# Performance work log

Measured on AMD Instinct MI355X. Metric: run time of the kernel, lower is better.

The kernel has to match this reference:

```python
import jax, jax.numpy as jnp
from jax import lax
import numpy as np

DN = ('NCDHW', 'OIDHW', 'NCDHW')
SLOPE = 0.01   # nn.LeakyReLU default negative_slope
EPS = 1e-5     # nn.BatchNorm1d default eps


def _conv(x, w, s, p):
    return lax.conv_general_dilated(x, w, (s, s, s), [(p, p)] * 3,
                                    dimension_numbers=DN)


def _tconv(x, w):
    # ConvTranspose3d(k=4, s=2, p=1) == conv with lhs_dilation=2,
    # pad = k-1-p = 2, spatially flipped kernel. w is (C_out, C_in, 4,4,4).
    return lax.conv_general_dilated(x, jnp.flip(w, (2, 3, 4)), (1, 1, 1),
                                    [(2, 2)] * 3, lhs_dilation=(2, 2, 2),
                                    dimension_numbers=DN)


def _bcast(v):
    return v[None, :, None, None, None]


def _masked_bn(y, m, g, b):
    # BatchNorm1d over ACTIVE voxels only (spconv stores only active sites).
    cnt = jnp.maximum(jnp.sum(m), 1.0)
    mean = jnp.sum(y * m, axis=(0, 2, 3, 4)) / cnt
    var = jnp.sum(jnp.square(y - _bcast(mean)) * m, axis=(0, 2, 3, 4)) / cnt
    yhat = (y - _bcast(mean)) * _bcast(lax.rsqrt(var + EPS))
    return (yhat * _bcast(g) + _bcast(b)) * m


def _block(x, m, w, b, g, be, transpose):
    # spconv SparseConv(Transpose)3d -> LeakyReLU -> BatchNorm1d, emulated
    # densely: x is zero off the active set m; output active set is the
    # dilation of m by the kernel footprint; bias/activation/BN touch only
    # active sites.
    ones_k = jnp.ones((1, 1, 4, 4, 4), x.dtype)
    if transpose:
        y = _tconv(x, w)
        m2 = (_tconv(m, ones_k) > 0).astype(x.dtype)
    else:
        y = _conv(x, w, 2, 1)
        m2 = (_conv(m, ones_k, 2, 1) > 0).astype(x.dtype)
    y = (y + _bcast(b)) * m2
    y = jnp.where(y >= 0, y, SLOPE * y)  # LeakyReLU (preserves zeros)
    return _masked_bn(y, m2, g, be), m2


def setup_inputs() -> dict:
    key = jax.random.key(0)
    ks = jax.random.split(key, 16)
    B, C, D = 2, 4, 64
    c = 32          # chans
    pred_dim = 32

    def w_init(k, shape):
        scale = 1.0 / float(np.sqrt(np.prod(shape[1:])))
        return jax.random.normal(k, shape, jnp.float32) * scale

    def b_init(k, n):
        return jax.random.normal(k, (n,), jnp.float32) * 0.01

    inp = {
        'feat': jax.random.normal(ks[0], (B, C, D, D, D), jnp.float32),
        'mask': jax.random.uniform(ks[1], (B, 1, D, D, D), jnp.float32),
        # down: [C->c, c->2c, 2c->4c], k=4 s=2 p=1
        'w1': w_init(ks[2], (c, C, 4, 4, 4)),
        'b1': b_init(ks[3], c),
        'g1': jnp.ones((c,), jnp.float32), 'be1': jnp.zeros((c,), jnp.float32),
        'w2': w_init(ks[4], (2 * c, c, 4, 4, 4)),
        'b2': b_init(ks[5], 2 * c),
        'g2': jnp.ones((2 * c,), jnp.float32), 'be2': jnp.zeros((2 * c,), jnp.float32),
        'w3': w_init(ks[6], (4 * c, 2 * c, 4, 4, 4)),
        'b3': b_init(ks[7], 4 * c),
        'g3': jnp.ones((4 * c,), jnp.float32), 'be3': jnp.zeros((4 * c,), jnp.float32),
        # up: [4c->4c, 4c->2c] (no skip-concat in the executed forward)
        'tw1': w_init(ks[8], (4 * c, 4 * c, 4, 4, 4)),
        'tb1': b_init(ks[9], 4 * c),
        'tg1': jnp.ones((4 * c,), jnp.float32), 'tbe1': jnp.zeros((4 * c,), jnp.float32),
        'tw2': w_init(ks[10], (2 * c, 4 * c, 4, 4, 4)),
        'tb2': b_init(ks[11], 2 * c),
        'tg2': jnp.ones((2 * c,), jnp.float32), 'tbe2': jnp.zeros((2 * c,), jnp.float32),
        # final dense 1x1x1 Conv3d: 2c -> pred_dim
        'fw': w_init(ks[12], (pred_dim, 2 * c, 1, 1, 1)),
        'fb': b_init(ks[13], pred_dim),
    }
    return inp


def reference(feat, mask, w1, b1, g1, be1, w2, b2, g2, be2, w3, b3, g3, be3,
              tw1, tb1, tg1, tbe1, tw2, tb2, tg2, tbe2, fw, fb):
    m = (mask > 0.5).astype(feat.dtype)
    x = feat * m  # gather of active voxel features == dense zero-fill
    x, m = _block(x, m, w1, b1, g1, be1, False)   # 64^3 -> 32^3
    x, m = _block(x, m, w2, b2, g2, be2, False)   # 32^3 -> 16^3
    x, m = _block(x, m, w3, b3, g3, be3, False)   # 16^3 -> 8^3
    x, m = _block(x, m, tw1, tb1, tg1, tbe1, True)  # 8^3 -> 16^3
    x, m = _block(x, m, tw2, tb2, tg2, tbe2, True)  # 16^3 -> 32^3
    # ToDense() then dense 1x1x1 Conv3d (bias applied everywhere)
    return _conv(x, fw, 1, 0) + _bcast(fb)
```

## Files before the change

### kernel.cpp

```cpp
#include <hip/hip_runtime.h>
#include <hip/hip_bf16.h>

#define DEV static __device__ __forceinline__

typedef unsigned short ushort;
typedef __attribute__((ext_vector_type(8))) short short8;
typedef __attribute__((ext_vector_type(8))) ushort ushort8;
typedef __attribute__((ext_vector_type(4))) ushort ushortx4;
typedef __attribute__((ext_vector_type(4))) float accv;

DEV ushort f2bf(float f) {
    __hip_bfloat16 h = __float2bfloat16(f);
    return reinterpret_cast<ushort&>(h);
}

__device__ float    g_sred[5 * 128 * 32];
__device__ float    g_y1[2097152];
__device__ __align__(16) ushort g_y1b[2097152];
__device__ float    g_m1[65536];
__device__ float    g_y2[524288];
__device__ __align__(16) ushort g_y2b[524288];
__device__ float    g_m2[8192];
__device__ float    g_y3[131072];
__device__ __align__(16) ushort g_y3b[131072];
__device__ float    g_m3[1024];
__device__ float    g_t1[1048576];
__device__ __align__(16) ushort g_t1b[1048576];
__device__ float    g_mt1[8192];
__device__ float    g_mt2[65536];
__device__ float    g_t2[4194304];
__device__ __align__(16) ushort g_x0b[2097152];
__device__ float    g_p2[4194304];
__device__ float    g_p3[4194304];
__device__ float    g_p4[8388608];
__device__ __align__(16) ushort g_wb1[8192];
__device__ __align__(16) ushort g_wb2[131072];
__device__ __align__(16) ushort g_wb3[524288];
__device__ __align__(16) ushort g_wb4[1048576];
__device__ __align__(16) ushort g_wb5[524288];
__device__ float    g_fwt[2048];

__global__ __launch_bounds__(256)
void prep_all_kernel(const float* __restrict__ w1, const float* __restrict__ fw,
                     const float* __restrict__ w2, const float* __restrict__ w3,
                     const float* __restrict__ tw1, const float* __restrict__ tw2,
                     const float* __restrict__ feat, const float* __restrict__ mask) {
    int blk = blockIdx.x, tid = threadIdx.x;
    if (blk < 96) {
        int idx = blk * 256 + tid;
        if (idx < 20480) g_sred[idx] = 0.f;
        if (idx < 8192) {
            int co = idx >> 8, r = idx & 255;
            int tap = r >> 2, ci = r & 3;
            g_wb1[idx] = f2bf(w1[co * 256 + ci * 64 + tap]);
        }
        if (idx < 2048) { int co = idx >> 6, kg = idx & 63; g_fwt[kg * 32 + co] = fw[idx]; }
    } else if (blk < 608) {
        int idx = (blk - 96) * 256 + tid;
        int co = idx / 2048, r = idx % 2048;
        int ci = r >> 6, tap = r & 63;
        g_wb2[(size_t)co * 2048 + tap * 32 + ci] = f2bf(w2[idx]);
    } else if (blk < 2656) {
        int idx = (blk - 608) * 256 + tid;
        int co = idx / 4096, r = idx % 4096;
        int ci = r >> 6, tap = r & 63;
        g_wb3[(size_t)co * 4096 + tap * 64 + ci] = f2bf(w3[idx]);
    } else if (blk < 6752) {
        int idx = (blk - 2656) * 256 + tid;
        int co = idx / 8192, r = idx % 8192;
        int ci = r >> 6, t64 = r & 63;
        int kd = t64 >> 4, kh = (t64 >> 2) & 3, kw = t64 & 3;
        int pd = (3 - kd) & 1, td = (3 - kd) >> 1;
        int ph = (3 - kh) & 1, th = (3 - kh) >> 1;
        int pw = (3 - kw) & 1, tw = (3 - kw) >> 1;
        int parity = pd * 4 + ph * 2 + pw, t = td * 4 + th * 2 + tw;
        g_wb4[(((size_t)parity * 128 + co) * 8 + t) * 128 + ci] = f2bf(tw1[idx]);
    } else if (blk < 8800) {
        int idx = (blk - 6752) * 256 + tid;
        int co = idx / 8192, r = idx % 8192;
        int ci = r >> 6, t64 = r & 63;
        int kd = t64 >> 4, kh = (t64 >> 2) & 3, kw = t64 & 3;
        int pd = (3 - kd) & 1, td = (3 - kd) >> 1;
        int ph = (3 - kh) & 1, th = (3 - kh) >> 1;
        int pw = (3 - kw) & 1, tw = (3 - kw) >> 1;
        int parity = pd * 4 + ph * 2 + pw, t = td * 4 + th * 2 + tw;
        g_wb5[(((size_t)parity * 64 + co) * 8 + t) * 128 + ci] = f2bf(tw2[idx]);
    } else if (blk < 10848) {
        int idx = (blk - 8800) * 256 + tid;
        int b = idx >> 18, v = idx & 0x3FFFF;
        float mv = mask[idx] > 0.5f ? 1.f : 0.f;
        ushort pk[4];
#pragma unroll
        for (int c = 0; c < 4; c++) pk[c] = f2bf(feat[((b * 4 + c) << 18) + v] * mv);
        *(ushortx4*)&g_x0b[(size_t)idx * 4] = (ushortx4){pk[0], pk[1], pk[2], pk[3]};
    } else {
        int idx = (blk - 10848) * 256 + tid;
        int b = idx >> 15, v = idx & 0x7FFF;
        int od = v >> 10, rem = v & 1023;
        int oh = rem >> 5, ow = rem & 31;
        const float* mp = mask + ((size_t)b << 18);
        float acc = 0.f;
        for (int kd = 0; kd < 4; kd++) {
            int id = 2 * od - 1 + kd;
            if ((unsigned)id >= 64u) continue;
            for (int kh = 0; kh < 4; kh++) {
                int ih = 2 * oh - 1 + kh;
                if ((unsigned)ih >= 64u) continue;
                const float* row = mp + ((size_t)id * 64 + ih) * 64;
                for (int kw = 0; kw < 4; kw++) {
                    int iw = 2 * ow - 1 + kw;
                    if ((unsigned)iw < 64u && row[iw] > 0.5f) acc += 1.f;
                }
            }
        }
        g_m1[idx] = acc > 0.f ? 1.f : 0.f;
    }
}

DEV void mask_down_blk(const float* mprev, float* mout, int logDin, int logDo, int blk) {
    int Din = 1 << logDin, Do = 1 << logDo;
    int idx = blk * 256 + threadIdx.x;
    int b = idx >> (3 * logDo), v = idx & ((1 << (3 * logDo)) - 1);
    int od = v >> (2 * logDo), rem = v & ((1 << (2 * logDo)) - 1);
    int oh = rem >> logDo, ow = rem & (Do - 1);
    const float* mp = mprev + ((size_t)b << (3 * logDin));
    float acc = 0.f;
    for (int kd = 0; kd < 4; kd++) {
        int id = 2 * od - 1 + kd;
        if ((unsigned)id >= (unsigned)Din) continue;
        for (int kh = 0; kh < 4; kh++) {
            int ih = 2 * oh - 1 + kh;
            if ((unsigned)ih >= (unsigned)Din) continue;
            const float* row = mp + ((size_t)id * Din + ih) * Din;
            for (int kw = 0; kw < 4; kw++) {
                int iw = 2 * ow - 1 + kw;
                if ((unsigned)iw < (unsigned)Din) acc += row[iw];
            }
        }
    }
    mout[idx] = acc > 0.f ? 1.f : 0.f;
}

DEV void mask_up_blk(const float* mprev, float* mout, int logDin, int logDo, int blk) {
    int Din = 1 << logDin, Do = 1 << logDo;
    int idx = blk * 256 + threadIdx.x;
    int b = idx >> (3 * logDo), v = idx & ((1 << (3 * logDo)) - 1);
    int od = v >> (2 * logDo), rem = v & ((1 << (2 * logDo)) - 1);
    int oh = rem >> logDo, ow = rem & (Do - 1);
    const float* mp = mprev + ((size_t)b << (3 * logDin));
    float acc = 0.f;
    for (int kd = 0; kd < 4; kd++) {
        int u = od + kd - 2; if (u < 0 || (u & 1)) continue;
        int id = u >> 1; if (id >= Din) continue;
        for (int kh = 0; kh < 4; kh++) {
            int uh = oh + kh - 2; if (uh < 0 || (uh & 1)) continue;
            int ih = uh >> 1; if (ih >= Din) continue;
            const float* row = mp + ((size_t)id * Din + ih) * Din;
            for (int kw = 0; kw < 4; kw++) {
                int uw = ow + kw - 2; if (uw < 0 || (uw & 1)) continue;
                int iw = uw >> 1; if (iw >= Din) continue;
                acc += row[iw];
            }
        }
    }
    mout[idx] = acc > 0.f ? 1.f : 0.f;
}

template<int MODE, int MT, int NT, int CIN, int COUT, int LOGDI, int LOGDO, int SPLITK>
DEV void mfma_gemm_body(const ushort* __restrict__ xb, const ushort* __restrict__ wb,
                        float* __restrict__ y) {
    constexpr int KT = 32;
    constexpr int K  = (MODE == 1) ? CIN * 8 : CIN * 64;
    constexpr int KSEG = K / SPLITK;
    constexpr int LDA = 40;
    constexpr int MTW = MT / 32, NTW = NT / 32;
    constexpr int AR = MT * 4 / 256, BR = NT * 4 / 256;
    constexpr int LCIN = (CIN == 32) ? 5 : ((CIN == 64) ? 6 : 7);
    constexpr int Din = 1 << LOGDI, Do = 1 << LOGDO;
    constexpr int DvoxI = 1 << (3 * LOGDI), DvoxO = 1 << (3 * LOGDO);

    __shared__ __align__(16) ushort As[MT * LDA];
    __shared__ __align__(16) ushort Bs[NT * LDA];

    const int tid = threadIdx.x;
    const int bx = blockIdx.x;
    int pd = 0, ph = 0, pw = 0, ks = 0;
    const ushort* wp = wb;
    if constexpr (MODE == 1) {
        int z = blockIdx.z;
        pd = (z >> 2) & 1; ph = (z >> 1) & 1; pw = z & 1; ks = z >> 3;
        wp = wb + (size_t)(z & 7) * COUT * CIN * 8;
    } else {
        ks = blockIdx.z;
    }

    const int wv = tid >> 6, lane = tid & 63;
    const int mw = wv & 1, nw = wv >> 1;
    const int lr = lane & 15, quad = lane >> 4;

    int rB[BR], dB[BR], hB[BR], wBv[BR];
#pragma unroll
    for (int r = 0; r < BR; r++) {
        int slot = r * 256 + tid;
        int n = slot >> 2;
        int vg = bx * NT + n;
        if constexpr (MODE == 0) {
            rB[r] = vg >> (3 * LOGDO);
            int vv = vg & (DvoxO - 1);
            dB[r] = 2 * (vv >> (2 * LOGDO)) - 1;
            hB[r] = 2 * ((vv >> LOGDO) & (Do - 1)) - 1;
            wBv[r] = 2 * (vv & (Do - 1)) - 1;
        } else {
            rB[r] = vg >> (3 * LOGDI);
            int vv = vg & (DvoxI - 1);
            dB[r] = (vv >> (2 * LOGDI)) + pd - 1;
            hB[r] = ((vv >> LOGDI) & (Din - 1)) + ph - 1;
            wBv[r] = (vv & (Din - 1)) + pw - 1;
        }
    }

    auto gatherA = [&](int kt, ushort8* pa) {
#pragma unroll
        for (int r = 0; r < AR; r++) {
            int slot = r * 256 + tid;
            int m = slot >> 2, oct = slot & 3;
            pa[r] = *(const ushort8*)&wp[(size_t)m * K + kt + oct * 8];
        }
    };
    auto gatherB = [&](int kt, ushort8* pb) {
        int tap = kt >> LCIN;
        int cib = kt & (CIN - 1);
        int id_d, ih_d, iw_d;
        if constexpr (MODE == 0) { id_d = tap >> 4; ih_d = (tap >> 2) & 3; iw_d = tap & 3; }
        else                     { id_d = (tap >> 2) & 1; ih_d = (tap >> 1) & 1; iw_d = tap & 1; }
#pragma unroll
        for (int r = 0; r < BR; r++) {
            int oct = (r * 256 + tid) & 3;
            int ci0 = cib + oct * 8;
            int id = dB[r] + id_d, ih = hB[r] + ih_d, iw = wBv[r] + iw_d;
            ushort8 v = (ushort8){0, 0, 0, 0, 0, 0, 0, 0};
            if ((unsigned)id < (unsigned)Din && (unsigned)ih < (unsigned)Din &&
                (unsigned)iw < (unsigned)Din)
                v = *(const ushort8*)&xb[((size_t)rB[r] * DvoxI +
                                          (id << (2 * LOGDI)) + (ih << LOGDI) + iw) * CIN + ci0];
            pb[r] = v;
        }
    };

    accv acc[MTW][NTW];
#pragma unroll
    for (int mt = 0; mt < MTW; mt++)
#pragma unroll
        for (int nt = 0; nt < NTW; nt++) acc[mt][nt] = (accv){0.f, 0.f, 0.f, 0.f};

    const int kbeg = ks * KSEG, kend = kbeg + KSEG;
    ushort8 pa[AR], pb[BR], qa[AR], qb[BR];
    gatherA(kbeg, pa);
    gatherB(kbeg, pb);

    for (int kt = kbeg; kt < kend; kt += KT) {
        __syncthreads();
#pragma unroll
        for (int r = 0; r < AR; r++) {
            int slot = r * 256 + tid;
            int m = slot >> 2, oct = slot & 3;
            *(ushort8*)&As[m * LDA + oct * 8] = pa[r];
        }
#pragma unroll
        for (int r = 0; r < BR; r++) {
            int slot = r * 256 + tid;
            int n = slot >> 2, oct = slot & 3;
            *(ushort8*)&Bs[n * LDA + oct * 8] = pb[r];
        }
        __syncthreads();
        bool more = (kt + KT) < kend;
        if (more) { gatherA(kt + KT, qa); gatherB(kt + KT, qb); }

        short8 af[MTW], bfr[NTW];
#pragma unroll
        for (int mt = 0; mt < MTW; mt++)
            af[mt] = *(const short8*)&As[((mw * MTW + mt) * 16 + lr) * LDA + quad * 8];
#pragma unroll
        for (int nt = 0; nt < NTW; nt++)
            bfr[nt] = *(const short8*)&Bs[((nw * NTW + nt) * 16 + lr) * LDA + quad * 8];
#pragma unroll
        for (int mt = 0; mt < MTW; mt++)
#pragma unroll
            for (int nt = 0; nt < NTW; nt++)
                acc[mt][nt] = __builtin_amdgcn_mfma_f32_16x16x32_bf16(
                    af[mt], bfr[nt], acc[mt][nt], 0, 0, 0);
        if (more) {
#pragma unroll
            for (int r = 0; r < AR; r++) pa[r] = qa[r];
#pragma unroll
            for (int r = 0; r < BR; r++) pb[r] = qb[r];
        }
    }

    float* yp = y + (size_t)ks * (2 * COUT * DvoxO);
#pragma unroll
    for (int mt = 0; mt < MTW; mt++) {
#pragma unroll
        for (int nt = 0; nt < NTW; nt++) {
#pragma unroll
            for (int r = 0; r < 4; r++) {
                int co = (mw * MTW + mt) * 16 + quad * 4 + r;
                int vg = bx * NT + (nw * NTW + nt) * 16 + lr;
                size_t idx;
                if constexpr (MODE == 1) {
                    int b = vg >> (3 * LOGDI);
                    int vv = vg & (DvoxI - 1);
                    int odp = vv >> (2 * LOGDI), ohp = (vv >> LOGDI) & (Din - 1), owp = vv & (Din - 1);
                    int od = 2 * odp + pd, oh = 2 * ohp + ph, ow = 2 * owp + pw;
                    idx = (((size_t)(b * COUT + co)) << (3 * LOGDO)) +
                          (od << (2 * LOGDO)) + (oh << LOGDO) + ow;
                } else {
                    int b = vg >> (3 * LOGDO);
                    int off = vg & (DvoxO - 1);
                    idx = (((size_t)(b * COUT + co)) << (3 * LOGDO)) + off;
                }
                yp[idx] = acc[mt][nt][r];
            }
        }
    }
}

__global__ __launch_bounds__(256)
void conv2_kernel() { mfma_gemm_body<0, 64, 128, 32, 64, 5, 4, 8>(g_y1b, g_wb2, g_p2); }
__global__ __launch_bounds__(256)
void conv3_kernel() { mfma_gemm_body<0, 128, 64, 64, 128, 4, 3, 32>(g_y2b, g_wb3, g_p3); }
__global__ __launch_bounds__(256)
void conv4_kernel() { mfma_gemm_body<1, 128, 128, 128, 128, 3, 4, 8>(g_y3b, g_wb4, g_p4); }
__global__ __launch_bounds__(256)
void conv5_kernel() { mfma_gemm_body<1, 64, 128, 128, 64, 4, 5, 1>(g_t1b, g_wb5, g_t2); }

__global__ __launch_bounds__(256)
void conv1_kernel(const float* __restrict__ bias) {
    constexpr int LDA = 40;
    __shared__ __align__(16) ushort As[32 * LDA];
    __shared__ __align__(16) ushort Bs[64 * LDA];
    const int tid = threadIdx.x, bx = blockIdx.x;
    const int wv = tid >> 6, lane = tid & 63;
    const int lr = lane & 15, quad = lane >> 4;

    const int nB = tid >> 2, octB = tid & 3;
    const int vgB = bx * 64 + nB;
    const int bB = vgB >> 15, vB = vgB & 32767;
    const int odB = vB >> 10, ohB = (vB >> 5) & 31, owB = vB & 31;

    auto gatherA = [&](int kt, ushort8& pa) {
        if (tid < 128) {
            int m = tid >> 2, oct = tid & 3;
            pa = *(const ushort8*)&g_wb1[m * 256 + kt + oct * 8];
        }
    };
    auto gatherB = [&](int kt, ushort8& pb) {
        int kg0 = kt + octB * 8;
        int t0 = kg0 >> 2;
        int kd = t0 >> 4, kh = (t0 >> 2) & 3, kw0 = t0 & 3;
        int id = 2 * odB - 1 + kd;
        int ih = 2 * ohB - 1 + kh;
        int iw0 = 2 * owB - 1 + kw0;
        ushort8 v = (ushort8){0, 0, 0, 0, 0, 0, 0, 0};
        if ((unsigned)id < 64u && (unsigned)ih < 64u) {
            const ushort* base = g_x0b + ((((size_t)bB << 18) + (id << 12) + (ih << 6)) << 2);
            if (iw0 >= 0 && iw0 + 1 < 64) {
                v = *(const ushort8*)&base[iw0 << 2];
            } else {
                if ((unsigned)iw0 < 64u) {
                    ushortx4 h = *(const ushortx4*)&base[iw0 << 2];
                    v[0] = h[0]; v[1] = h[1]; v[2] = h[2]; v[3] = h[3];
                }
                if ((unsigned)(iw0 + 1) < 64u) {
                    ushortx4 h = *(const ushortx4*)&base[(iw0 + 1) << 2];
                    v[4] = h[0]; v[5] = h[1]; v[6] = h[2]; v[7] = h[3];
                }
            }
        }
        pb = v;
    };

    accv acc[2];
    acc[0] = (accv){0.f, 0.f, 0.f, 0.f};
    acc[1] = (accv){0.f, 0.f, 0.f, 0.f};
    ushort8 pa, pb, qa, qb;
    gatherA(0, pa); gatherB(0, pb);

    for (int kt = 0; kt < 256; kt += 32) {
        __syncthreads();
        if (tid < 128) { int m = tid >> 2, oct = tid & 3; *(ushort8*)&As[m * LDA + oct * 8] = pa; }
        *(ushort8*)&Bs[nB * LDA + octB * 8] = pb;
        __syncthreads();
        bool more = kt < 224;
        if (more) { gatherA(kt + 32, qa); gatherB(kt + 32, qb); }

        short8 b8 = *(const short8*)&Bs[(wv * 16 + lr) * LDA + quad * 8];
#pragma unroll
        for (int mt = 0; mt < 2; mt++) {
            short8 a8 = *(const short8*)&As[(mt * 16 + lr) * LDA + quad * 8];
            acc[mt] = __builtin_amdgcn_mfma_f32_16x16x32_bf16(a8, b8, acc[mt], 0, 0, 0);
        }
        if (more) { pa = qa; pb = qb; }
    }

#pragma unroll
    for (int mt = 0; mt < 2; mt++) {
#pragma unroll
        for (int r = 0; r < 4; r++) {
            int co = mt * 16 + quad * 4 + r;
            int vg = bx * 64 + wv * 16 + lr;
            int b = vg >> 15, off = vg & 32767;
            float mv = g_m1[((size_t)b << 15) + off];
            float yv = (acc[mt][r] + bias[co]) * mv;
            yv = yv >= 0.f ? yv : 0.01f * yv;
            g_y1[(((size_t)(b * 32 + co)) << 15) + off] = yv;
        }
    }
}

__global__ __launch_bounds__(256)
void final_kernel(const float* __restrict__ fb, const float* __restrict__ b5,
                  const float* __restrict__ tg2, const float* __restrict__ tbe2,
                  float* __restrict__ out) {
    __shared__ float As[1024];
    __shared__ float Bs[2048];
    __shared__ float sc5[64], sh5[64], bb5[64];
    const int tid = threadIdx.x, tc = tid & 15, tv = tid >> 4;
    const int bx = blockIdx.x;

    if (tid < 64) {
        const float* sred = g_sred + 16384;
        float n = fmaxf(sred[tid * 32 + 2], 1.f);
        float mean = sred[tid * 32] / n;
        float var = fmaxf(sred[tid * 32 + 1] / n - mean * mean, 0.f);
        float rstd = rsqrtf(var + 1e-5f);
        float s = tg2[tid] * rstd;
        sc5[tid] = s; sh5[tid] = tbe2[tid] - mean * s; bb5[tid] = b5[tid];
    }

    float acc[2][4] = {{0.f}};
    for (int kt = 0; kt < 64; kt += 32) {
        __syncthreads();
#pragma unroll
        for (int e = 0; e < 4; e++) As[e * 256 + tid] = g_fwt[kt * 32 + e * 256 + tid];
#pragma unroll
        for (int e = 0; e < 8; e++) {
            int j = e * 256 + tid;
            int kk = j >> 6, n = j & 63;
            int kg = kt + kk;
            int vg = bx * 64 + n;
            int b = vg >> 15, v = vg & 32767;
            float raw = g_t2[(((size_t)(b * 64 + kg)) << 15) + v];
            float mv = g_mt2[((size_t)b << 15) + v];
            float t = (raw + bb5[kg]) * mv;
            t = t >= 0.f ? t : 0.01f * t;
            Bs[kk * 64 + n] = (t * sc5[kg] + sh5[kg]) * mv;
        }
        __syncthreads();
#pragma unroll
        for (int kk = 0; kk < 32; kk++) {
            float2 a2 = *(const float2*)&As[kk * 32 + tc * 2];
            float4 b4 = *(const float4*)&Bs[kk * 64 + tv * 4];
            float a[2] = {a2.x, a2.y};
            float bb[4] = {b4.x, b4.y, b4.z, b4.w};
#pragma unroll
            for (int r = 0; r < 2; r++)
#pragma unroll
                for (int c = 0; c < 4; c++) acc[r][c] = fmaf(a[r], bb[c], acc[r][c]);
        }
    }
#pragma unroll
    for (int r = 0; r < 2; r++) {
        int co = tc * 2 + r;
        float bv = fb[co];
#pragma unroll
        for (int c = 0; c < 4; c++) {
            int vg = bx * 64 + tv * 4 + c;
            int b = vg >> 15, v = vg & 32767;
            out[(((size_t)(b * 32 + co)) << 15) + v] = acc[r][c] + bv;
        }
    }
}

DEV void red3_and_atomic(float s, float s2, float sm, float* sred, int co) {
#pragma unroll
    for (int off = 32; off; off >>= 1) {
        s  += __shfl_down(s, off, 64);
        s2 += __shfl_down(s2, off, 64);
        sm += __shfl_down(sm, off, 64);
    }
    __shared__ float red[12];
    int lane = threadIdx.x & 63, wvi = threadIdx.x >> 6;
    if (!lane) { red[wvi] = s; red[4 + wvi] = s2; red[8 + wvi] = sm; }
    __syncthreads();
    if (!threadIdx.x) {
        atomicAdd(&sred[co * 32 + 0], red[0] + red[1] + red[2] + red[3]);
        atomicAdd(&sred[co * 32 + 1], red[4] + red[5] + red[6] + red[7]);
        atomicAdd(&sred[co * 32 + 2], red[8] + red[9] + red[10] + red[11]);
    }
}

template<int COUT, int LOGDO, int SPLITK, int ITERS, bool WRITE>
DEV void post_body(const float* __restrict__ bias, const float* __restrict__ m2,
                   const float* p, float* y, float* sred) {
    constexpr int Dvox = 1 << (3 * LOGDO);
    constexpr size_t STR = (size_t)2 * COUT * Dvox;
    constexpr int LOGC = (COUT == 128) ? 7 : ((COUT == 64) ? 6 : 5);
    int base = blockIdx.x * (ITERS * 256);
    int co = (base >> (3 * LOGDO)) & (COUT - 1);
    float s = 0.f, s2 = 0.f, sm = 0.f;
#pragma unroll
    for (int it = 0; it < ITERS; it++) {
        int idx = base + it * 256 + threadIdx.x;
        int v = idx & (Dvox - 1);
        int b = idx >> (3 * LOGDO + LOGC);
        float sum = 0.f;
#pragma unroll
        for (int k = 0; k < SPLITK; k++) sum += p[k * STR + idx];
        float mv = m2[((size_t)b << (3 * LOGDO)) + v];
        float yv = (sum + bias[co]) * mv;
        yv = yv >= 0.f ? yv : 0.01f * yv;
        if constexpr (WRITE) y[idx] = yv;
        s += yv; s2 += yv * yv; sm += mv;
    }
    red3_and_atomic(s, s2, sm, sred, co);
}

__global__ __launch_bounds__(256) void post2_kernel(const float* b) { post_body<64, 4, 8, 1, true>(b, g_m2, g_p2, g_y2, g_sred + 4096); }
__global__ __launch_bounds__(256) void post3_kernel(const float* b) { post_body<128, 3, 32, 1, true>(b, g_m3, g_p3, g_y3, g_sred + 8192); }
__global__ __launch_bounds__(256) void post4_kernel(const float* b) { post_body<128, 4, 8, 2, true>(b, g_mt1, g_p4, g_t1, g_sred + 12288); }
__global__ __launch_bounds__(256) void post5_kernel(const float* b) { post_body<64, 5, 1, 8, false>(b, g_mt2, g_t2, g_t2, g_sred + 16384); }

__global__ __launch_bounds__(256)
void stats1_kernel() {
    int base = blockIdx.x * 1024;
    int co = (base >> 15) & 31;
    float s = 0.f, s2 = 0.f, sm = 0.f;
#pragma unroll
    for (int it = 0; it < 4; it++) {
        int idx = base + it * 256 + threadIdx.x;
        int v = idx & 32767;
        int b = idx >> 20;
        float yv = g_y1[idx];
        float mv = g_m1[((size_t)b << 15) + v];
        s += yv; s2 += yv * yv; sm += mv;
    }
    red3_and_atomic(s, s2, sm, g_sred, co);
}

template<int LOGC, int LOGD>
DEV void bn_fused_body(const float* __restrict__ y, ushort* __restrict__ out,
                       const float* __restrict__ sred, const float* __restrict__ gm,
                       const float* __restrict__ be, const float* __restrict__ m2,
                       int blk) {
    constexpr int C = 1 << LOGC, Dvox = 1 << LOGD;
    __shared__ float sc[C], sh[C];
    int tid = threadIdx.x;
    if (tid < C) {
        float n = fmaxf(sred[tid * 32 + 2], 1.f);
        float mean = sred[tid * 32] / n;
        float var = fmaxf(sred[tid * 32 + 1] / n - mean * mean, 0.f);
        float rstd = rsqrtf(var + 1e-5f);
        float s = gm[tid] * rstd;
        sc[tid] = s; sh[tid] = be[tid] - mean * s;
    }
    __syncthreads();
    int gv = blk * 256 + tid;
    int b = gv >> LOGD, vox = gv & (Dvox - 1);
    float mv = m2[gv];
    const float* yp = y + (((size_t)b << LOGC) << LOGD) + vox;
    ushort* op = out + (size_t)gv * C;
#pragma unroll
    for (int c0 = 0; c0 < C; c0 += 8) {
        ushort pk[8];
#pragma unroll
        for (int j = 0; j < 8; j++) {
            int c = c0 + j;
            float val = yp[(size_t)c << LOGD];
            pk[j] = f2bf((val * sc[c] + sh[c]) * mv);
        }
        *(ushort8*)&op[c0] = (ushort8){pk[0], pk[1], pk[2], pk[3], pk[4], pk[5], pk[6], pk[7]};
    }
}

__global__ __launch_bounds__(256)
void bn1_kernel(const float* g, const float* be) {
    if (blockIdx.x < 256) bn_fused_body<5, 15>(g_y1, g_y1b, g_sred + 0, g, be, g_m1, blockIdx.x);
    else mask_down_blk(g_m1, g_m2, 5, 4, blockIdx.x - 256);
}
__global__ __launch_bounds__(256)
void bn2_kernel(const float* g, const float* be) {
    if (blockIdx.x < 32) bn_fused_body<6, 12>(g_y2, g_y2b, g_sred + 4096, g, be, g_m2, blockIdx.x);
    else mask_down_blk(g_m2, g_m3, 4, 3, blockIdx.x - 32);
}
__global__ __launch_bounds__(256)
void bn3_kernel(const float* g, const float* be) {
    if (blockIdx.x < 4) bn_fused_body<7, 9>(g_y3, g_y3b, g_sred + 8192, g, be, g_m3, blockIdx.x);
    else mask_up_blk(g_m3, g_mt1, 3, 4, blockIdx.x - 4);
}
__global__ __launch_bounds__(256)
void bn4_kernel(const float* g, const float* be) {
    if (blockIdx.x < 32) bn_fused_body<7, 12>(g_t1, g_t1b, g_sred + 12288, g, be, g_mt1, blockIdx.x);
    else mask_up_blk(g_mt1, g_mt2, 4, 5, blockIdx.x - 32);
}


extern "C" void kernel_launch(void* const* d_in, const int* in_sizes, int n_in,
                              void* d_out, int out_size, void* d_ws, size_t ws_size,
                              hipStream_t stream) {
    (void)in_sizes; (void)n_in; (void)out_size; (void)d_ws; (void)ws_size;
    const float* feat = (const float*)d_in[0];
    const float* mask = (const float*)d_in[1];
    const float* w1  = (const float*)d_in[2];
    const float* b1  = (const float*)d_in[3];
    const float* g1  = (const float*)d_in[4];
    const float* be1 = (const float*)d_in[5];
    const float* w2  = (const float*)d_in[6];
    const float* b2  = (const float*)d_in[7];
    const float* g2  = (const float*)d_in[8];
    const float* be2 = (const float*)d_in[9];
    const float* w3  = (const float*)d_in[10];
    const float* b3  = (const float*)d_in[11];
    const float* g3  = (const float*)d_in[12];
    const float* be3 = (const float*)d_in[13];
    const float* tw1 = (const float*)d_in[14];
    const float* tb1 = (const float*)d_in[15];
    const float* tg1 = (const float*)d_in[16];
    const float* tbe1= (const float*)d_in[17];
    const float* tw2 = (const float*)d_in[18];
    const float* tb2 = (const float*)d_in[19];
    const float* tg2 = (const float*)d_in[20];
    const float* tbe2= (const float*)d_in[21];
    const float* fw  = (const float*)d_in[22];
    const float* fb  = (const float*)d_in[23];

    prep_all_kernel<<<11104, 256, 0, stream>>>(w1, fw, w2, w3, tw1, tw2, feat, mask);

    conv1_kernel<<<1024, 256, 0, stream>>>(b1);
    stats1_kernel<<<2048, 256, 0, stream>>>();
    bn1_kernel<<<288, 256, 0, stream>>>(g1, be1);

    conv2_kernel<<<dim3(64, 1, 8), 256, 0, stream>>>();
    post2_kernel<<<2048, 256, 0, stream>>>(b2);
    bn2_kernel<<<36, 256, 0, stream>>>(g2, be2);

    conv3_kernel<<<dim3(16, 1, 32), 256, 0, stream>>>();
    post3_kernel<<<512, 256, 0, stream>>>(b3);
    bn3_kernel<<<36, 256, 0, stream>>>(g3, be3);

    conv4_kernel<<<dim3(8, 1, 64), 256, 0, stream>>>();
    post4_kernel<<<2048, 256, 0, stream>>>(tb1);
    bn4_kernel<<<288, 256, 0, stream>>>(tg1, tbe1);

    conv5_kernel<<<dim3(64, 1, 8), 256, 0, stream>>>();
    post5_kernel<<<2048, 256, 0, stream>>>(tb2);

    final_kernel<<<1024, 256, 0, stream>>>(fb, tb2, tg2, tbe2, (float*)d_out);
}
```

Before: 278.6 us.

## Fuse BN statistics into conv epilogues and drop separate stats/post kernels

Folds the per-channel sum, sum-of-squares and mask-count reductions into the conv1 and conv5 epilogues, which removes the stats1 and post5 kernels and their extra passes over the activations. Conv5 now also applies bias and LeakyReLU, so final_kernel only applies the BN affine. Atomic accumulation is spread over 8 sub-slots to reduce contention, with the mask count moved to a separate buffer. Weight-prep loops are rewritten to write outputs contiguously while gathering from the inputs. The cost is more epilogue work and atomics inside the GEMM kernels.

```diff
diff --git a/kernel.cpp b/kernel.cpp
--- a/kernel.cpp
+++ b/kernel.cpp
@@ -15,6 +15,7 @@
 }
 
 __device__ float    g_sred[5 * 128 * 32];
+__device__ float    g_mcnt[160];
 __device__ float    g_y1[2097152];
 __device__ __align__(16) ushort g_y1b[2097152];
 __device__ float    g_m1[65536];
@@ -49,6 +50,7 @@
     if (blk < 96) {
         int idx = blk * 256 + tid;
         if (idx < 20480) g_sred[idx] = 0.f;
+        if (idx < 160)   g_mcnt[idx] = 0.f;
         if (idx < 8192) {
             int co = idx >> 8, r = idx & 255;
             int tap = r >> 2, ci = r & 3;
@@ -57,34 +59,32 @@
         if (idx < 2048) { int co = idx >> 6, kg = idx & 63; g_fwt[kg * 32 + co] = fw[idx]; }
     } else if (blk < 608) {
         int idx = (blk - 96) * 256 + tid;
-        int co = idx / 2048, r = idx % 2048;
-        int ci = r >> 6, tap = r & 63;
-        g_wb2[(size_t)co * 2048 + tap * 32 + ci] = f2bf(w2[idx]);
+        int co = idx >> 11, rem = idx & 2047;
+        int tap = rem >> 5, ci = rem & 31;
+        g_wb2[idx] = f2bf(w2[co * 2048 + ci * 64 + tap]);
     } else if (blk < 2656) {
         int idx = (blk - 608) * 256 + tid;
-        int co = idx / 4096, r = idx % 4096;
-        int ci = r >> 6, tap = r & 63;
-        g_wb3[(size_t)co * 4096 + tap * 64 + ci] = f2bf(w3[idx]);
+        int co = idx >> 12, rem = idx & 4095;
+        int tap = rem >> 6, ci = rem & 63;
+        g_wb3[idx] = f2bf(w3[co * 4096 + ci * 64 + tap]);
     } else if (blk < 6752) {
         int idx = (blk - 2656) * 256 + tid;
-        int co = idx / 8192, r = idx % 8192;
-        int ci = r >> 6, t64 = r & 63;
-        int kd = t64 >> 4, kh = (t64 >> 2) & 3, kw = t64 & 3;
-        int pd = (3 - kd) & 1, td = (3 - kd) >> 1;
-        int ph = (3 - kh) & 1, th = (3 - kh) >> 1;
-        int pw = (3 - kw) & 1, tw = (3 - kw) >> 1;
-        int parity = pd * 4 + ph * 2 + pw, t = td * 4 + th * 2 + tw;
-        g_wb4[(((size_t)parity * 128 + co) * 8 + t) * 128 + ci] = f2bf(tw1[idx]);
+        int parity = idx >> 17, rem = idx & 0x1FFFF;
+        int co = rem >> 10, rem2 = rem & 1023;
+        int t = rem2 >> 7, ci = rem2 & 127;
+        int td = (t >> 2) & 1, th = (t >> 1) & 1, tw = t & 1;
+        int pd = (parity >> 2) & 1, ph = (parity >> 1) & 1, pw = parity & 1;
+        int kd = 3 - 2 * td - pd, kh = 3 - 2 * th - ph, kw = 3 - 2 * tw - pw;
+        g_wb4[idx] = f2bf(tw1[co * 8192 + ci * 64 + kd * 16 + kh * 4 + kw]);
     } else if (blk < 8800) {
         int idx = (blk - 6752) * 256 + tid;
-        int co = idx / 8192, r = idx % 8192;
-        int ci = r >> 6, t64 = r & 63;
-        int kd = t64 >> 4, kh = (t64 >> 2) & 3, kw = t64 & 3;
-        int pd = (3 - kd) & 1, td = (3 - kd) >> 1;
-        int ph = (3 - kh) & 1, th = (3 - kh) >> 1;
-        int pw = (3 - kw) & 1, tw = (3 - kw) >> 1;
-        int parity = pd * 4 + ph * 2 + pw, t = td * 4 + th * 2 + tw;
-        g_wb5[(((size_t)parity * 64 + co) * 8 + t) * 128 + ci] = f2bf(tw2[idx]);
+        int parity = idx >> 16, rem = idx & 0xFFFF;
+        int co = rem >> 10, rem2 = rem & 1023;
+        int t = rem2 >> 7, ci = rem2 & 127;
+        int td = (t >> 2) & 1, th = (t >> 1) & 1, tw = t & 1;
+        int pd = (parity >> 2) & 1, ph = (parity >> 1) & 1, pw = parity & 1;
+        int kd = 3 - 2 * td - pd, kh = 3 - 2 * th - ph, kw = 3 - 2 * tw - pw;
+        g_wb5[idx] = f2bf(tw2[co * 8192 + ci * 64 + kd * 16 + kh * 4 + kw]);
     } else if (blk < 10848) {
         int idx = (blk - 8800) * 256 + tid;
         int b = idx >> 18, v = idx & 0x3FFFF;
@@ -166,9 +166,11 @@
     mout[idx] = acc > 0.f ? 1.f : 0.f;
 }
 
-template<int MODE, int MT, int NT, int CIN, int COUT, int LOGDI, int LOGDO, int SPLITK>
+template<int MODE, int MT, int NT, int CIN, int COUT, int LOGDI, int LOGDO, int SPLITK, int EPI>
 DEV void mfma_gemm_body(const ushort* __restrict__ xb, const ushort* __restrict__ wb,
-                        float* __restrict__ y) {
+                        float* __restrict__ y, const float* __restrict__ bias,
+                        const float* __restrict__ m2s, float* __restrict__ sredL,
+                        float* __restrict__ mcntL) {
     constexpr int KT = 32;
     constexpr int K  = (MODE == 1) ? CIN * 8 : CIN * 64;
     constexpr int KSEG = K / SPLITK;
@@ -181,6 +183,7 @@
 
     __shared__ __align__(16) ushort As[MT * LDA];
     __shared__ __align__(16) ushort Bs[NT * LDA];
+    __shared__ float sb[(EPI == 1) ? COUT : 1];
 
     const int tid = threadIdx.x;
     const int bx = blockIdx.x;
@@ -193,6 +196,8 @@
     } else {
         ks = blockIdx.z;
     }
+
+    if constexpr (EPI == 1) { if (tid < COUT) sb[tid] = bias[tid]; }
 
     const int wv = tid >> 6, lane = tid & 63;
     const int mw = wv & 1, nw = wv >> 1;
@@ -297,48 +302,109 @@
         }
     }
 
-    float* yp = y + (size_t)ks * (2 * COUT * DvoxO);
-#pragma unroll
-    for (int mt = 0; mt < MTW; mt++) {
+    if constexpr (EPI == 0) {
+        float* yp = y + (size_t)ks * (2 * COUT * DvoxO);
+#pragma unroll
+        for (int mt = 0; mt < MTW; mt++) {
+#pragma unroll
+            for (int nt = 0; nt < NTW; nt++) {
+#pragma unroll
+                for (int r = 0; r < 4; r++) {
+                    int co = (mw * MTW + mt) * 16 + quad * 4 + r;
+                    int vg = bx * NT + (nw * NTW + nt) * 16 + lr;
+                    size_t idx;
+                    if constexpr (MODE == 1) {
+                        int b = vg >> (3 * LOGDI);
+                        int vv = vg & (DvoxI - 1);
+                        int odp = vv >> (2 * LOGDI), ohp = (vv >> LOGDI) & (Din - 1), owp = vv & (Din - 1);
+                        int od = 2 * odp + pd, oh = 2 * ohp + ph, ow = 2 * owp + pw;
+                        idx = (((size_t)(b * COUT + co)) << (3 * LOGDO)) +
+                              (od << (2 * LOGDO)) + (oh << LOGDO) + ow;
+                    } else {
+                        int b = vg >> (3 * LOGDO);
+                        int off = vg & (DvoxO - 1);
+                        idx = (((size_t)(b * COUT + co)) << (3 * LOGDO)) + off;
+                    }
+                    yp[idx] = acc[mt][nt][r];
+                }
+            }
+        }
+    } else {
+        __shared__ float sS[COUT][2], sQ[COUT][2], sM[2];
+        float sum_[MTW][4], ssq_[MTW][4];
+#pragma unroll
+        for (int mt = 0; mt < MTW; mt++)
+#pragma unroll
+            for (int r = 0; r < 4; r++) { sum_[mt][r] = 0.f; ssq_[mt][r] = 0.f; }
+        float smv = 0.f;
 #pragma unroll
         for (int nt = 0; nt < NTW; nt++) {
-#pragma unroll
-            for (int r = 0; r < 4; r++) {
-                int co = (mw * MTW + mt) * 16 + quad * 4 + r;
-                int vg = bx * NT + (nw * NTW + nt) * 16 + lr;
-                size_t idx;
-                if constexpr (MODE == 1) {
-                    int b = vg >> (3 * LOGDI);
-                    int vv = vg & (DvoxI - 1);
-                    int odp = vv >> (2 * LOGDI), ohp = (vv >> LOGDI) & (Din - 1), owp = vv & (Din - 1);
-                    int od = 2 * odp + pd, oh = 2 * ohp + ph, ow = 2 * owp + pw;
-                    idx = (((size_t)(b * COUT + co)) << (3 * LOGDO)) +
-                          (od << (2 * LOGDO)) + (oh << LOGDO) + ow;
-                } else {
-                    int b = vg >> (3 * LOGDO);
-                    int off = vg & (DvoxO - 1);
-                    idx = (((size_t)(b * COUT + co)) << (3 * LOGDO)) + off;
+            int vg = bx * NT + (nw * NTW + nt) * 16 + lr;
+            int b = vg >> (3 * LOGDI);
+            int vv = vg & (DvoxI - 1);
+            int odp = vv >> (2 * LOGDI), ohp = (vv >> LOGDI) & (Din - 1), owp = vv & (Din - 1);
+            int od = 2 * odp + pd, oh = 2 * ohp + ph, ow = 2 * owp + pw;
+            size_t off = (od << (2 * LOGDO)) + (oh << LOGDO) + ow;
+            float mv = m2s[((size_t)b << (3 * LOGDO)) + off];
+            if (quad == 0) smv += mv;
+#pragma unroll
+            for (int mt = 0; mt < MTW; mt++) {
+#pragma unroll
+                for (int r = 0; r < 4; r++) {
+                    int co = (mw * MTW + mt) * 16 + quad * 4 + r;
+                    float yv = (acc[mt][nt][r] + sb[co]) * mv;
+                    yv = yv >= 0.f ? yv : 0.01f * yv;
+                    y[(((size_t)(b * COUT + co)) << (3 * LOGDO)) + off] = yv;
+                    sum_[mt][r] += yv; ssq_[mt][r] += yv * yv;
                 }
-                yp[idx] = acc[mt][nt][r];
             }
         }
-    }
-}
-
-__global__ __launch_bounds__(256)
-void conv2_kernel() { mfma_gemm_body<0, 64, 128, 32, 64, 5, 4, 8>(g_y1b, g_wb2, g_p2); }
-__global__ __launch_bounds__(256)
-void conv3_kernel() { mfma_gemm_body<0, 128, 64, 64, 128, 4, 3, 32>(g_y2b, g_wb3, g_p3); }
-__global__ __launch_bounds__(256)
-void conv4_kernel() { mfma_gemm_body<1, 128, 128, 128, 128, 3, 4, 8>(g_y3b, g_wb4, g_p4); }
-__global__ __launch_bounds__(256)
-void conv5_kernel() { mfma_gemm_body<1, 64, 128, 128, 64, 4, 5, 1>(g_t1b, g_wb5, g_t2); }
+#pragma unroll
+        for (int mt = 0; mt < MTW; mt++)
+#pragma unroll
+            for (int r = 0; r < 4; r++)
+#pragma unroll
+                for (int o = 8; o; o >>= 1) {
+                    sum_[mt][r] += __shfl_down(sum_[mt][r], o, 16);
+                    ssq_[mt][r] += __shfl_down(ssq_[mt][r], o, 16);
+                }
+#pragma unroll
+        for (int o = 8; o; o >>= 1) smv += __shfl_down(smv, o, 16);
+        if (lr == 0) {
+#pragma unroll
+            for (int mt = 0; mt < MTW; mt++)
+#pragma unroll
+                for (int r = 0; r < 4; r++) {
+                    int co = (mw * MTW + mt) * 16 + quad * 4 + r;
+                    sS[co][nw] = sum_[mt][r]; sQ[co][nw] = ssq_[mt][r];
+                }
+            if (quad == 0 && mw == 0) sM[nw] = smv;
+        }
+        __syncthreads();
+        int sub = (bx + blockIdx.z) & 7;
+        if (tid < COUT) {
+            atomicAdd(&sredL[tid * 32 + sub * 3],     sS[tid][0] + sS[tid][1]);
+            atomicAdd(&sredL[tid * 32 + sub * 3 + 1], sQ[tid][0] + sQ[tid][1]);
+        }
+        if (tid == COUT) atomicAdd(&mcntL[sub * 4], sM[0] + sM[1]);
+    }
+}
+
+__global__ __launch_bounds__(256)
+void conv2_kernel() { mfma_gemm_body<0, 64, 128, 32, 64, 5, 4, 8, 0>(g_y1b, g_wb2, g_p2, nullptr, nullptr, nullptr, nullptr); }
+__global__ __launch_bounds__(256)
+void conv3_kernel() { mfma_gemm_body<0, 128, 64, 64, 128, 4, 3, 32, 0>(g_y2b, g_wb3, g_p3, nullptr, nullptr, nullptr, nullptr); }
+__global__ __launch_bounds__(256)
+void conv4_kernel() { mfma_gemm_body<1, 128, 128, 128, 128, 3, 4, 8, 0>(g_y3b, g_wb4, g_p4, nullptr, nullptr, nullptr, nullptr); }
+__global__ __launch_bounds__(256)
+void conv5_kernel(const float* b5) { mfma_gemm_body<1, 64, 128, 128, 64, 4, 5, 1, 1>(g_t1b, g_wb5, g_t2, b5, g_mt2, g_sred + 16384, g_mcnt + 128); }
 
 __global__ __launch_bounds__(256)
 void conv1_kernel(const float* __restrict__ bias) {
     constexpr int LDA = 40;
     __shared__ __align__(16) ushort As[32 * LDA];
     __shared__ __align__(16) ushort Bs[64 * LDA];
+    __shared__ float sS[32][4], sQ[32][4], sM[4];
     const int tid = threadIdx.x, bx = blockIdx.x;
     const int wv = tid >> 6, lane = tid & 63;
     const int lr = lane & 15, quad = lane >> 4;
@@ -403,39 +469,77 @@
         if (more) { pa = qa; pb = qb; }
     }
 
+    int vg = bx * 64 + wv * 16 + lr;
+    int b = vg >> 15, off = vg & 32767;
+    float mv = g_m1[((size_t)b << 15) + off];
+    float sum_[2][4], ssq_[2][4];
 #pragma unroll
     for (int mt = 0; mt < 2; mt++) {
 #pragma unroll
         for (int r = 0; r < 4; r++) {
             int co = mt * 16 + quad * 4 + r;
-            int vg = bx * 64 + wv * 16 + lr;
-            int b = vg >> 15, off = vg & 32767;
-            float mv = g_m1[((size_t)b << 15) + off];
             float yv = (acc[mt][r] + bias[co]) * mv;
             yv = yv >= 0.f ? yv : 0.01f * yv;
             g_y1[(((size_t)(b * 32 + co)) << 15) + off] = yv;
-        }
-    }
-}
-
-__global__ __launch_bounds__(256)
-void final_kernel(const float* __restrict__ fb, const float* __restrict__ b5,
-                  const float* __restrict__ tg2, const float* __restrict__ tbe2,
-                  float* __restrict__ out) {
+            sum_[mt][r] = yv; ssq_[mt][r] = yv * yv;
+        }
+    }
+    float smv = (quad == 0) ? mv : 0.f;
+#pragma unroll
+    for (int mt = 0; mt < 2; mt++)
+#pragma unroll
+        for (int r = 0; r < 4; r++)
+#pragma unroll
+            for (int o = 8; o; o >>= 1) {
+                sum_[mt][r] += __shfl_down(sum_[mt][r], o, 16);
+                ssq_[mt][r] += __shfl_down(ssq_[mt][r], o, 16);
+            }
+#pragma unroll
+    for (int o = 8; o; o >>= 1) smv += __shfl_down(smv, o, 16);
+    if (lr == 0) {
+#pragma unroll
+        for (int mt = 0; mt < 2; mt++)
+#pragma unroll
+            for (int r = 0; r < 4; r++) {
+                int co = mt * 16 + quad * 4 + r;
+                sS[co][wv] = sum_[mt][r]; sQ[co][wv] = ssq_[mt][r];
+            }
+        if (quad == 0) sM[wv] = smv;
+    }
+    __syncthreads();
+    int sub = bx & 7;
+    if (tid < 32) {
+        atomicAdd(&g_sred[tid * 32 + sub * 3],     sS[tid][0] + sS[tid][1] + sS[tid][2] + sS[tid][3]);
+        atomicAdd(&g_sred[tid * 32 + sub * 3 + 1], sQ[tid][0] + sQ[tid][1] + sQ[tid][2] + sQ[tid][3]);
+    }
+    if (tid == 32) atomicAdd(&g_mcnt[sub * 4], sM[0] + sM[1] + sM[2] + sM[3]);
+}
+
+__global__ __launch_bounds__(256)
+void final_kernel(const float* __restrict__ fb, const float* __restrict__ tg2,
+                  const float* __restrict__ tbe2, float* __restrict__ out) {
     __shared__ float As[1024];
     __shared__ float Bs[2048];
-    __shared__ float sc5[64], sh5[64], bb5[64];
+    __shared__ float sc5[64], sh5[64];
     const int tid = threadIdx.x, tc = tid & 15, tv = tid >> 4;
     const int bx = blockIdx.x;
 
     if (tid < 64) {
         const float* sred = g_sred + 16384;
-        float n = fmaxf(sred[tid * 32 + 2], 1.f);
-        float mean = sred[tid * 32] / n;
-        float var = fmaxf(sred[tid * 32 + 1] / n - mean * mean, 0.f);
+        const float* mc = g_mcnt + 128;
+        float n = 0.f, su = 0.f, sq = 0.f;
+#pragma unroll
+        for (int s = 0; s < 8; s++) {
+            n += mc[s * 4];
+            su += sred[tid * 32 + s * 3];
+            sq += sred[tid * 32 + s * 3 + 1];
+        }
+        n = fmaxf(n, 1.f);
+        float mean = su / n;
+        float var = fmaxf(sq / n - mean * mean, 0.f);
         float rstd = rsqrtf(var + 1e-5f);
         float s = tg2[tid] * rstd;
-        sc5[tid] = s; sh5[tid] = tbe2[tid] - mean * s; bb5[tid] = b5[tid];
+        sc5[tid] = s; sh5[tid] = tbe2[tid] - mean * s;
     }
 
     float acc[2][4] = {{0.f}};
@@ -452,9 +556,7 @@
             int b = vg >> 15, v = vg & 32767;
             float raw = g_t2[(((size_t)(b * 64 + kg)) << 15) + v];
             float mv = g_mt2[((size_t)b << 15) + v];
-            float t = (raw + bb5[kg]) * mv;
-            t = t >= 0.f ? t : 0.01f * t;
-            Bs[kk * 64 + n] = (t * sc5[kg] + sh5[kg]) * mv;
+            Bs[kk * 64 + n] = (raw * sc5[kg] + sh5[kg]) * mv;
         }
         __syncthreads();
 #pragma unroll
@@ -482,7 +584,8 @@
     }
 }
 
-DEV void red3_and_atomic(float s, float s2, float sm, float* sred, int co) {
+DEV void red_stats(float s, float s2, float sm, float* sred, float* mcnt,
+                   int co, int sub, bool doMask) {
 #pragma unroll
     for (int off = 32; off; off >>= 1) {
         s  += __shfl_down(s, off, 64);
@@ -494,15 +597,15 @@
     if (!lane) { red[wvi] = s; red[4 + wvi] = s2; red[8 + wvi] = sm; }
     __syncthreads();
     if (!threadIdx.x) {
-        atomicAdd(&sred[co * 32 + 0], red[0] + red[1] + red[2] + red[3]);
-        atomicAdd(&sred[co * 32 + 1], red[4] + red[5] + red[6] + red[7]);
-        atomicAdd(&sred[co * 32 + 2], red[8] + red[9] + red[10] + red[11]);
-    }
-}
-
-template<int COUT, int LOGDO, int SPLITK, int ITERS, bool WRITE>
+        atomicAdd(&sred[co * 32 + sub * 3],     red[0] + red[1] + red[2] + red[3]);
+        atomicAdd(&sred[co * 32 + sub * 3 + 1], red[4] + red[5] + red[6] + red[7]);
+        if (doMask) atomicAdd(&mcnt[sub * 4],   red[8] + red[9] + red[10] + red[11]);
+    }
+}
+
+template<int COUT, int LOGDO, int SPLITK, int ITERS>
 DEV void post_body(const float* __restrict__ bias, const float* __restrict__ m2,
-                   const float* p, float* y, float* sred) {
+                   const float* p, float* y, float* sred, float* mcnt) {
     constexpr int Dvox = 1 << (3 * LOGDO);
     constexpr size_t STR = (size_t)2 * COUT * Dvox;
     constexpr int LOGC = (COUT == 128) ? 7 : ((COUT == 64) ? 6 : 5);
@@ -520,46 +623,35 @@
         float mv = m2[((size_t)b << (3 * LOGDO)) + v];
         float yv = (sum + bias[co]) * mv;
         yv = yv >= 0.f ? yv : 0.01f * yv;
-        if constexpr (WRITE) y[idx] = yv;
+        y[idx] = yv;
         s += yv; s2 += yv * yv; sm += mv;
     }
-    red3_and_atomic(s, s2, sm, sred, co);
-}
-
-__global__ __launch_bounds__(256) void post2_kernel(const float* b) { post_body<64, 4, 8, 1, true>(b, g_m2, g_p2, g_y2, g_sred + 4096); }
-__global__ __launch_bounds__(256) void post3_kernel(const float* b) { post_body<128, 3, 32, 1, true>(b, g_m3, g_p3, g_y3, g_sred + 8192); }
-__global__ __launch_bounds__(256) void post4_kernel(const float* b) { post_body<128, 4, 8, 2, true>(b, g_mt1, g_p4, g_t1, g_sred + 12288); }
-__global__ __launch_bounds__(256) void post5_kernel(const float* b) { post_body<64, 5, 1, 8, false>(b, g_mt2, g_t2, g_t2, g_sred + 16384); }
-
-__global__ __launch_bounds__(256)
-void stats1_kernel() {
-    int base = blockIdx.x * 1024;
-    int co = (base >> 15) & 31;
-    float s = 0.f, s2 = 0.f, sm = 0.f;
-#pragma unroll
-    for (int it = 0; it < 4; it++) {
-        int idx = base + it * 256 + threadIdx.x;
-        int v = idx & 32767;
-        int b = idx >> 20;
-        float yv = g_y1[idx];
-        float mv = g_m1[((size_t)b << 15) + v];
-        s += yv; s2 += yv * yv; sm += mv;
-    }
-    red3_and_atomic(s, s2, sm, g_sred, co);
-}
+    red_stats(s, s2, sm, sred, mcnt, co, blockIdx.x & 7, co == 0);
+}
+
+__global__ __launch_bounds__(256) void post2_kernel(const float* b) { post_body<64, 4, 8, 1>(b, g_m2, g_p2, g_y2, g_sred + 4096, g_mcnt + 32); }
+__global__ __launch_bounds__(256) void post3_kernel(const float* b) { post_body<128, 3, 32, 1>(b, g_m3, g_p3, g_y3, g_sred + 8192, g_mcnt + 64); }
+__global__ __launch_bounds__(256) void post4_kernel(const float* b) { post_body<128, 4, 8, 2>(b, g_mt1, g_p4, g_t1, g_sred + 12288, g_mcnt + 96); }
 
 template<int LOGC, int LOGD>
 DEV void bn_fused_body(const float* __restrict__ y, ushort* __restrict__ out,
-                       const float* __restrict__ sred, const float* __restrict__ gm,
-                       const float* __restrict__ be, const float* __restrict__ m2,
-                       int blk) {
+                       const float* __restrict__ sred, const float* __restrict__ mcnt,
+                       const float* __restrict__ gm, const float* __restrict__ be,
+                       const float* __restrict__ m2, int blk) {
     constexpr int C = 1 << LOGC, Dvox = 1 << LOGD;
     __shared__ float sc[C], sh[C];
     int tid = threadIdx.x;
     if (tid < C) {
-        float n = fmaxf(sred[tid * 32 + 2], 1.f);
-        float mean = sred[tid * 32] / n;
-        float var = fmaxf(sred[tid * 32 + 1] / n - mean * mean, 0.f);
+        float n = 0.f, su = 0.f, sq = 0.f;
+#pragma unroll
+        for (int s = 0; s < 8; s++) {
+            n += mcnt[s * 4];
+            su += sred[tid * 32 + s * 3];
+            sq += sred[tid * 32 + s * 3 + 1];
+        }
+        n = fmaxf(n, 1.f);
+        float mean = su / n;
+        float var = fmaxf(sq / n - mean * mean, 0.f);
         float rstd = rsqrtf(var + 1e-5f);
         float s = gm[tid] * rstd;
         sc[tid] = s; sh[tid] = be[tid] - mean * s;
@@ -585,22 +677,22 @@
 
 __global__ __launch_bounds__(256)
 void bn1_kernel(const float* g, const float* be) {
-    if (blockIdx.x < 256) bn_fused_body<5, 15>(g_y1, g_y1b, g_sred + 0, g, be, g_m1, blockIdx.x);
+    if (blockIdx.x < 256) bn_fused_body<5, 15>(g_y1, g_y1b, g_sred + 0, g_mcnt + 0, g, be, g_m1, blockIdx.x);
     else mask_down_blk(g_m1, g_m2, 5, 4, blockIdx.x - 256);
 }
 __global__ __launch_bounds__(256)
 void bn2_kernel(const float* g, const float* be) {
-    if (blockIdx.x < 32) bn_fused_body<6, 12>(g_y2, g_y2b, g_sred + 4096, g, be, g_m2, blockIdx.x);
+    if (blockIdx.x < 32) bn_fused_body<6, 12>(g_y2, g_y2b, g_sred + 4096, g_mcnt + 32, g, be, g_m2, blockIdx.x);
     else mask_down_blk(g_m2, g_m3, 4, 3, blockIdx.x - 32);
 }
 __global__ __launch_bounds__(256)
 void bn3_kernel(const float* g, const float* be) {
-    if (blockIdx.x < 4) bn_fused_body<7, 9>(g_y3, g_y3b, g_sred + 8192, g, be, g_m3, blockIdx.x);
+    if (blockIdx.x < 4) bn_fused_body<7, 9>(g_y3, g_y3b, g_sred + 8192, g_mcnt + 64, g, be, g_m3, blockIdx.x);
     else mask_up_blk(g_m3, g_mt1, 3, 4, blockIdx.x - 4);
 }
 __global__ __launch_bounds__(256)
 void bn4_kernel(const float* g, const float* be) {
-    if (blockIdx.x < 32) bn_fused_body<7, 12>(g_t1, g_t1b, g_sred + 12288, g, be, g_mt1, blockIdx.x);
+    if (blockIdx.x < 32) bn_fused_body<7, 12>(g_t1, g_t1b, g_sred + 12288, g_mcnt + 96, g, be, g_mt1, blockIdx.x);
     else mask_up_blk(g_mt1, g_mt2, 4, 5, blockIdx.x - 32);
 }
 
@@ -637,7 +729,6 @@
     prep_all_kernel<<<11104, 256, 0, stream>>>(w1, fw, w2, w3, tw1, tw2, feat, mask);
 
     conv1_kernel<<<1024, 256, 0, stream>>>(b1);
-    stats1_kernel<<<2048, 256, 0, stream>>>();
     bn1_kernel<<<288, 256, 0, stream>>>(g1, be1);
 
     conv2_kernel<<<dim3(64, 1, 8), 256, 0, stream>>>();
@@ -652,8 +743,7 @@
     post4_kernel<<<2048, 256, 0, stream>>>(tb1);
     bn4_kernel<<<288, 256, 0, stream>>>(tg1, tbe1);
 
-    conv5_kernel<<<dim3(64, 1, 8), 256, 0, stream>>>();
-    post5_kernel<<<2048, 256, 0, stream>>>(tb2);
-
-    final_kernel<<<1024, 256, 0, stream>>>(fb, tb2, tg2, tbe2, (float*)d_out);
-}
+    conv5_kernel<<<dim3(64, 1, 8), 256, 0, stream>>>(tb2);
+
+    final_kernel<<<1024, 256, 0, stream>>>(fb, tg2, tbe2, (float*)d_out);
+}
```

Measured after the change: 300.0 us. 7.7% more time.
